# Kernel optimization log

Hardware: AMD Instinct MI355X
Metric: run time of the kernel (lower is better)

The kernel has to match this reference:

```python
import jax, jax.numpy as jnp
import numpy as np

B, T, E, D, N, L, NF = 4, 2048, 512, 512, 16, 4, 2048


def setup_inputs() -> dict:
    key = jax.random.key(0)
    ks = jax.random.split(key, 12)
    r = lambda k, s, sc=1.0: jax.random.normal(k, s, dtype=jnp.float32) * sc
    return {
        "text_emb": r(ks[0], (B, T, E)),
        "W_in": r(ks[1], (E, D), 1.0 / np.sqrt(E).astype(np.float32)),
        "b_in": jnp.zeros((D,), jnp.float32),
        "freq_pe": r(ks[2], (NF, D), 0.02),
        # diagonal-SSM (S4D) params per layer, stacked on leading L axis
        "A_log": r(ks[3], (L, D, N), 0.5),
        "B_ssm": r(ks[4], (L, D, N), 0.5),
        "C_ssm": r(ks[5], (L, D, N), 0.5),
        "log_dt": r(ks[6], (L, D), 0.5) - 4.6,  # dt ~ 0.01
        "D_skip": r(ks[7], (L, D), 0.5),
        "ln_f0_scale": jnp.ones((D,), jnp.float32),
        "ln_f0_bias": jnp.zeros((D,), jnp.float32),
        "W_f0": r(ks[8], (D, 1), 1.0 / np.sqrt(D).astype(np.float32)),
        "b_f0": jnp.zeros((1,), jnp.float32),
        "ln_en_scale": jnp.ones((D,), jnp.float32),
        "ln_en_bias": jnp.zeros((D,), jnp.float32),
        "W_en": r(ks[9], (D, 1), 1.0 / np.sqrt(D).astype(np.float32)),
        "b_en": jnp.zeros((1,), jnp.float32),
    }


def _layernorm(x, scale, bias, eps=1e-5):
    mu = jnp.mean(x, axis=-1, keepdims=True)
    var = jnp.mean(jnp.square(x - mu), axis=-1, keepdims=True)
    return (x - mu) * jax.lax.rsqrt(var + eps) * scale + bias


def _s4_layer(h, A_log, Bm, Cm, log_dt, Dsk):
    # h: [B, T, D]; diagonal SSM with ZOH discretization, scanned over T.
    dt = jnp.exp(log_dt)                 # [D]
    A = -jnp.exp(A_log)                  # [D, N], stable (negative real)
    Abar = jnp.exp(dt[:, None] * A)      # [D, N]
    Bbar = (Abar - 1.0) / A * Bm         # [D, N]
    u_t = jnp.transpose(h, (1, 0, 2))    # [T, B, D]
    x0 = jnp.zeros((h.shape[0], h.shape[2], A.shape[1]), h.dtype)  # [B, D, N]

    def step(x, u):
        x = Abar * x + Bbar * u[..., None]          # [B, D, N]
        y = jnp.einsum('bdn,dn->bd', x, Cm)         # readout
        return x, y

    _, ys = jax.lax.scan(step, x0, u_t)             # ys: [T, B, D]
    y = jnp.transpose(ys, (1, 0, 2)) + Dsk * h      # D skip connection
    return h + jax.nn.gelu(y)                       # residual + activation


def _forward(text_emb, W_in, b_in, freq_pe, A_log, B_ssm, C_ssm, log_dt,
             D_skip, ln_f0_scale, ln_f0_bias, W_f0, b_f0,
             ln_en_scale, ln_en_bias, W_en, b_en):
    x = text_emb @ W_in + b_in                      # [B, T, D]
    Tlen = x.shape[1]
    nf = freq_pe.shape[0]
    if nf >= Tlen:                                  # static-shape crop
        freq = freq_pe[:Tlen]
    else:                                           # static-shape edge pad
        pad = jnp.repeat(freq_pe[-1:], Tlen - nf, axis=0)
        freq = jnp.concatenate([freq_pe, pad], axis=0)
    h = x + freq[None, :, :]
    for l in range(A_log.shape[0]):
        h = _s4_layer(h, A_log[l], B_ssm[l], C_ssm[l], log_dt[l], D_skip[l])
    f0 = (_layernorm(h, ln_f0_scale, ln_f0_bias) @ W_f0 + b_f0)[..., 0]
    en = (_layernorm(h, ln_en_scale, ln_en_bias) @ W_en + b_en)[..., 0]
    return f0, en


def reference(text_emb, W_in, b_in, freq_pe, A_log, B_ssm, C_ssm, log_dt,
              D_skip, ln_f0_scale, ln_f0_bias, W_f0, b_f0,
              ln_en_scale, ln_en_bias, W_en, b_en):
    return _forward(text_emb, W_in, b_in, freq_pe, A_log, B_ssm, C_ssm,
                    log_dt, D_skip, ln_f0_scale, ln_f0_bias, W_f0, b_f0,
                    ln_en_scale, ln_en_bias, W_en, b_en)
```

## Files before the change

### kernel.cpp

```cpp
#include <hip/hip_runtime.h>

#define B_   4
#define T_   2048
#define E_   512
#define D_   512
#define N_   16
#define L_   4
#define TCH  32

typedef __bf16 bf16x8 __attribute__((ext_vector_type(8)));
typedef float  f32x4  __attribute__((ext_vector_type(4)));
typedef float  f32x2  __attribute__((ext_vector_type(2)));
typedef unsigned short us8 __attribute__((ext_vector_type(8)));

__device__ __forceinline__ float us2f(unsigned short u) {
    return __uint_as_float(((unsigned int)u) << 16);
}
__device__ __forceinline__ unsigned short f2us(float f) {
    unsigned int u = __float_as_uint(f);
    unsigned int r = (u + 0x7fffu + ((u >> 16) & 1u)) >> 16;
    return (unsigned short)r;
}
__device__ __forceinline__ float ldin(const void* p, int i, unsigned int f) {
    return f ? ((const float*)p)[i] : us2f(((const unsigned short*)p)[i]);
}
__device__ __forceinline__ unsigned int probe_f32(const void* lnfs) {
    return (((const unsigned int*)lnfs)[0] == 0x3F800000u) ? 1u : 0u;
}
__device__ __forceinline__ f32x2 pk_fma(f32x2 a, f32x2 b, f32x2 c) {
    f32x2 d;
    asm("v_pk_fma_f32 %0, %1, %2, %3" : "=v"(d) : "v"(a), "v"(b), "v"(c));
    return d;
}
template<int CTRL, int RM>
__device__ __forceinline__ f32x2 dpp2(f32x2 v) {
    f32x2 r;
    r[0] = __int_as_float(__builtin_amdgcn_update_dpp(0, __float_as_int(v[0]), CTRL, RM, 0xF, true));
    r[1] = __int_as_float(__builtin_amdgcn_update_dpp(0, __float_as_int(v[1]), CTRL, RM, 0xF, true));
    return r;
}
template<int CTRL>
__device__ __forceinline__ f32x2 mdpp2(f32x2 v) {
    f32x2 r;
    r[0] = __int_as_float(__builtin_amdgcn_mov_dpp(__float_as_int(v[0]), CTRL, 0xF, 0xF, true));
    r[1] = __int_as_float(__builtin_amdgcn_mov_dpp(__float_as_int(v[1]), CTRL, 0xF, 0xF, true));
    return r;
}

#define PA    0
#define PB    32768
#define PC    65536
#define PDT   98304
#define PDSK  100352
#define PLFS  102400
#define PLFB  102912
#define PWF   103424
#define PLES  103936
#define PLEB  104448
#define PWEN  104960
#define PSC   105472
#define PRM_N 105474

#define NB_TEXT 2048
#define NB_PRM  413
#define NB_WT   64
#define NB_S4P  128

__global__ __launch_bounds__(256) void prep_kernel(
    const void* X, const void* Win,
    const void* A_log, const void* B_ssm, const void* C_ssm,
    const void* log_dt, const void* D_skip,
    const void* lnfs, const void* lnfb, const void* Wf0,
    const void* lnes, const void* lneb, const void* Wen,
    const void* bf0, const void* ben,
    unsigned short* __restrict__ textc, unsigned short* __restrict__ Wt,
    float* __restrict__ P, float* __restrict__ P2, float* __restrict__ PW) {
    __shared__ float tile[64 * 65];
    unsigned int f = probe_f32(lnfs);
    int bid = blockIdx.x;
    if (bid < NB_TEXT) {
        int i = (bid * 256 + threadIdx.x) * 8;
        if (f) {
            const float* xf = (const float*)X;
            us8 r;
#pragma unroll
            for (int j = 0; j < 8; j++) r[j] = f2us(xf[i + j]);
            *(us8*)(textc + i) = r;
        } else {
            *(us8*)(textc + i) = *(const us8*)((const unsigned short*)X + i);
        }
    } else if (bid < NB_TEXT + NB_PRM) {
        int i = (bid - NB_TEXT) * 256 + threadIdx.x;
        if      (i < PB)     P[i] = ldin(A_log,  i - PA,   f);
        else if (i < PC)     P[i] = ldin(B_ssm,  i - PB,   f);
        else if (i < PDT)    P[i] = ldin(C_ssm,  i - PC,   f);
        else if (i < PDSK)   P[i] = ldin(log_dt, i - PDT,  f);
        else if (i < PLFS)   P[i] = ldin(D_skip, i - PDSK, f);
        else if (i < PLFB)   P[i] = ldin(lnfs,   i - PLFS, f);
        else if (i < PWF)    P[i] = ldin(lnfb,   i - PLFB, f);
        else if (i < PLES)   P[i] = ldin(Wf0,    i - PWF,  f);
        else if (i < PLEB)   P[i] = ldin(lnes,   i - PLES, f);
        else if (i < PWEN)   P[i] = ldin(lneb,   i - PLEB, f);
        else if (i < PSC)    P[i] = ldin(Wen,    i - PWEN, f);
        else if (i == PSC)     P[i] = ldin(bf0, 0, f);
        else if (i == PSC + 1) P[i] = ldin(ben, 0, f);
    } else if (bid < NB_TEXT + NB_PRM + NB_WT) {
        int tb = bid - (NB_TEXT + NB_PRM);
        int d0 = (tb >> 3) * 64, e0 = (tb & 7) * 64;
        int r = threadIdx.x >> 6, i = threadIdx.x & 63;
#pragma unroll
        for (int k = 0; k < 16; k++) {
            int e = k * 4 + r;
            tile[e * 65 + i] = ldin(Win, (e0 + e) * D_ + d0 + i, f);
        }
        __syncthreads();
#pragma unroll
        for (int k = 0; k < 16; k++) {
            int dd = k * 4 + r;
            Wt[(size_t)(d0 + dd) * E_ + e0 + i] = f2us(tile[i * 65 + dd]);
        }
    } else {
        int i = (bid - (NB_TEXT + NB_PRM + NB_WT)) * 256 + threadIdx.x;
        int n = i & 15;
        int ld = i >> 4;
        float dt = __expf(ldin(log_dt, ld, f));
        float A  = -__expf(ldin(A_log, i, f));
        float Ab = __expf(dt * A);
        float Bb = (Ab - 1.f) / A * ldin(B_ssm, i, f);
        float l2M = 46.166241308446827f * dt * A;
        float M   = exp2f(l2M);
        int base = ld * 32 + n;
        P2[base]      = Ab;
        P2[base + 16] = Bb * ldin(C_ssm, i, f);
        float pw = 1.f;
        size_t pb = ((size_t)ld << 10) + n;
#pragma unroll
        for (int k = 0; k < 33; k++) { PW[pb + (k << 4)] = pw; pw *= M; }
    }
}

__global__ __launch_bounds__(256) void gemm_kernel(const unsigned short* __restrict__ X,
                                                   const unsigned short* __restrict__ Wt,
                                                   const void* __restrict__ freq,
                                                   const void* __restrict__ b_in,
                                                   const void* __restrict__ lnfs,
                                                   float* __restrict__ H) {
    __shared__ unsigned short wlds[64 * 264];
    const unsigned int fl = probe_f32(lnfs);
    const int tid = threadIdx.x;
    const int w  = tid >> 6;
    const int ln = tid & 15;
    const int q  = (tid >> 4) & 3;
    const int d0 = blockIdx.x * 64;
    const int t0 = blockIdx.y * 64;
    const int b  = blockIdx.z;

    f32x4 acc[4];
#pragma unroll
    for (int j = 0; j < 4; j++) { acc[j][0]=0.f; acc[j][1]=0.f; acc[j][2]=0.f; acc[j][3]=0.f; }

    const size_t xbase = ((size_t)b * T_ + t0) * E_;

#pragma unroll
    for (int p = 0; p < 2; ++p) {
        if (p) __syncthreads();
#pragma unroll
        for (int it = 0; it < 8; ++it) {
            int flat = it * 256 + tid;
            int d = flat >> 5;
            int e = (flat & 31) << 3;
            bf16x8 v = *(const bf16x8*)(Wt + (size_t)(d0 + d) * E_ + p * 256 + e);
            *(bf16x8*)(wlds + d * 264 + e) = v;
        }
        __syncthreads();
#pragma unroll
        for (int s = 0; s < 8; ++s) {
            const int eo = s * 32 + q * 8;
            bf16x8 bfr[4];
#pragma unroll
            for (int j = 0; j < 4; j++)
                bfr[j] = *(const bf16x8*)(wlds + (j * 16 + ln) * 264 + eo);
            const int t = w * 16 + ln;
            bf16x8 afr = *(const bf16x8*)(X + xbase + (size_t)t * E_ + p * 256 + eo);
#pragma unroll
            for (int j = 0; j < 4; j++)
                acc[j] = __builtin_amdgcn_mfma_f32_16x16x32_bf16(afr, bfr[j], acc[j], 0, 0, 0);
        }
    }
#pragma unroll
    for (int j = 0; j < 4; j++) {
        int d  = d0 + j * 16 + ln;
        int tb = t0 + w * 16 + q * 4;
        float bi = ldin(b_in, d, fl);
        f32x4 o;
#pragma unroll
        for (int r4 = 0; r4 < 4; r4++)
            o[r4] = acc[j][r4] + ldin(freq, (tb + r4) * D_ + d, fl) + bi;
        *(f32x4*)(H + ((size_t)b * D_ + d) * T_ + tb) = o;
    }
}

__global__ __launch_bounds__(256, 2)
void s4_kernel(float* __restrict__ H, const float* __restrict__ P,
               const float* __restrict__ P2, const float* __restrict__ PW) {
    const int w = threadIdx.x >> 6, lane = threadIdx.x & 63;
    const int d = blockIdx.x;
    const int row = w * D_ + d;
    float* gp = H + (size_t)row * T_ + lane * TCH;

    float u[TCH];
#pragma unroll
    for (int k = 0; k < TCH / 4; k++) {
        f32x4 v = *(const f32x4*)(gp + k * 4);
        u[k * 4] = v[0]; u[k * 4 + 1] = v[1]; u[k * 4 + 2] = v[2]; u[k * 4 + 3] = v[3];
    }

    for (int l = 0; l < L_; ++l) {
        const float* pp  = P2 + (size_t)((l << 9) + d) * 32;
        const float* pwt = PW + ((size_t)((l << 9) + d) << 10);
        f32x2 b[8];
#pragma unroll
        for (int n = 0; n < 8; n++) { b[n][0] = 0.f; b[n][1] = 0.f; }
        {
            f32x2 Ab[8];
#pragma unroll
            for (int n = 0; n < 8; n++) Ab[n] = *(const f32x2*)(pp + 2 * n);
#pragma unroll
            for (int j = 0; j < TCH; j++) {
                f32x2 u2; u2[0] = u[j]; u2[1] = u[j];
#pragma unroll
                for (int n = 0; n < 8; n++) b[n] = pk_fma(Ab[n], b[n], u2);
            }
        }
        {
            f32x2 W[8];
#pragma unroll
            for (int n = 0; n < 8; n++) W[n] = *(const f32x2*)(pwt + 16 + 2 * n);
#pragma unroll
            for (int n = 0; n < 8; n++) b[n] = pk_fma(W[n], mdpp2<0x111>(b[n]), b[n]);
#pragma unroll
            for (int n = 0; n < 8; n++) W[n] = *(const f32x2*)(pwt + 32 + 2 * n);
#pragma unroll
            for (int n = 0; n < 8; n++) b[n] = pk_fma(W[n], mdpp2<0x112>(b[n]), b[n]);
#pragma unroll
            for (int n = 0; n < 8; n++) W[n] = *(const f32x2*)(pwt + 64 + 2 * n);
#pragma unroll
            for (int n = 0; n < 8; n++) b[n] = pk_fma(W[n], mdpp2<0x114>(b[n]), b[n]);
#pragma unroll
            for (int n = 0; n < 8; n++) W[n] = *(const f32x2*)(pwt + 128 + 2 * n);
#pragma unroll
            for (int n = 0; n < 8; n++) b[n] = pk_fma(W[n], mdpp2<0x118>(b[n]), b[n]);
        }
        {
            f32x2 w1[8];
            const float* p1 = pwt + (((lane & 15) + 1) << 4);
#pragma unroll
            for (int n = 0; n < 8; n++) w1[n] = *(const f32x2*)(p1 + 2 * n);
#pragma unroll
            for (int n = 0; n < 8; n++) b[n] = pk_fma(w1[n], dpp2<0x142, 0xA>(b[n]), b[n]);
        }
        {
            f32x2 w2[8];
            const float* p2_ = pwt + (((lane & 31) + 1) << 4);
#pragma unroll
            for (int n = 0; n < 8; n++) w2[n] = *(const f32x2*)(p2_ + 2 * n);
#pragma unroll
            for (int n = 0; n < 8; n++) b[n] = pk_fma(w2[n], dpp2<0x143, 0xC>(b[n]), b[n]);
        }
        f32x2 z[8];
#pragma unroll
        for (int n = 0; n < 8; n++) z[n] = mdpp2<0x138>(b[n]);
        float Dsk = P[PDSK + l * D_ + d];
        f32x2 Ab[8], CB[8];
#pragma unroll
        for (int n = 0; n < 8; n++) Ab[n] = *(const f32x2*)(pp + 2 * n);
#pragma unroll
        for (int n = 0; n < 8; n++) CB[n] = *(const f32x2*)(pp + 16 + 2 * n);
#pragma unroll
        for (int j = 0; j < TCH; j++) {
            float uu = u[j];
            f32x2 u2; u2[0] = uu; u2[1] = uu;
#pragma unroll
            for (int n = 0; n < 8; n++) z[n] = pk_fma(Ab[n], z[n], u2);
            f32x2 ya; ya[0] = 0.f; ya[1] = 0.f;
            f32x2 yb; yb[0] = 0.f; yb[1] = 0.f;
#pragma unroll
            for (int n = 0; n < 8; n += 2) {
                ya = pk_fma(CB[n], z[n], ya);
                yb = pk_fma(CB[n + 1], z[n + 1], yb);
            }
            f32x2 s = ya + yb;
            float y = fmaf(Dsk, uu, s[0] + s[1]);
            float t  = fmaf(0.044715f, y * y * y, y);
            float em = exp2f(-2.30220818f * t);
            float r  = __builtin_amdgcn_rcpf(1.f + em);
            u[j] = fmaf(y, r, uu);
        }
    }
#pragma unroll
    for (int k = 0; k < TCH / 4; k++) {
        f32x4 v;
        v[0] = u[k * 4]; v[1] = u[k * 4 + 1]; v[2] = u[k * 4 + 2]; v[3] = u[k * 4 + 3];
        *(f32x4*)(gp + k * 4) = v;
    }
}

__global__ __launch_bounds__(256) void final_kernel(const float* __restrict__ H,
                                                    const float* __restrict__ P,
                                                    void* __restrict__ out,
                                                    const void* __restrict__ lnfs_raw) {
    __shared__ float red[4][8][32];
    unsigned int f = probe_f32(lnfs_raw);
    int tid = threadIdx.x;
    int w = tid >> 6, lane = tid & 63;
    int tq = lane & 31, dp = lane >> 5;
    int tg = blockIdx.x * 32 + tq;
    int b = tg >> 11, t = tg & (T_ - 1);
    float S1=0.f,S2=0.f,Pf=0.f,Pe=0.f,Cf=0.f,Ce=0.f,Df=0.f,De=0.f;
    const float* hp = H + ((size_t)b * D_) * T_ + t;
#pragma unroll 4
    for (int k = 0; k < 64; k++) {
        int d = w * 128 + 2 * k + dp;
        float hv = hp[(size_t)d * T_];
        float sf = P[PLFS + d], bfv = P[PLFB + d], wf = P[PWF + d];
        float se = P[PLES + d], bev = P[PLEB + d], we = P[PWEN + d];
        S1 += hv; S2 = fmaf(hv, hv, S2);
        float tf = sf * wf, te = se * we;
        Pf = fmaf(hv, tf, Pf); Pe = fmaf(hv, te, Pe);
        Cf += tf; Ce += te;
        Df = fmaf(bfv, wf, Df); De = fmaf(bev, we, De);
    }
    S1 += __shfl_xor(S1, 32); S2 += __shfl_xor(S2, 32);
    Pf += __shfl_xor(Pf, 32); Pe += __shfl_xor(Pe, 32);
    Cf += __shfl_xor(Cf, 32); Ce += __shfl_xor(Ce, 32);
    Df += __shfl_xor(Df, 32); De += __shfl_xor(De, 32);
    if (dp == 0) {
        red[w][0][tq]=S1; red[w][1][tq]=S2; red[w][2][tq]=Pf; red[w][3][tq]=Pe;
        red[w][4][tq]=Cf; red[w][5][tq]=Ce; red[w][6][tq]=Df; red[w][7][tq]=De;
    }
    __syncthreads();
    if (tid < 32) {
        float a[8];
#pragma unroll
        for (int k = 0; k < 8; k++)
            a[k] = red[0][k][tid] + red[1][k][tid] + red[2][k][tid] + red[3][k][tid];
        float mu  = a[0] * (1.f / 512.f);
        float var = a[1] * (1.f / 512.f) - mu * mu;
        float r   = rsqrtf(var + 1e-5f);
        float f0  = r * (a[2] - mu * a[4]) + a[6] + P[PSC + 0];
        float en  = r * (a[3] - mu * a[5]) + a[7] + P[PSC + 1];
        int tg2 = blockIdx.x * 32 + tid;
        if (f) {
            ((float*)out)[tg2]           = f0;
            ((float*)out)[B_ * T_ + tg2] = en;
        } else {
            ((unsigned short*)out)[tg2]           = f2us(f0);
            ((unsigned short*)out)[B_ * T_ + tg2] = f2us(en);
        }
    }
}

extern "C" void kernel_launch(void* const* d_in, const int* in_sizes, int n_in,
                              void* d_out, int out_size, void* d_ws, size_t ws_size,
                              hipStream_t stream) {
    (void)in_sizes; (void)n_in; (void)out_size; (void)ws_size;
    float* ws = (float*)d_ws;
    float* P     = ws;
    float* H     = ws + 105504;
    unsigned short* textc = (unsigned short*)(ws + 4299808);
    unsigned short* Wt    = (unsigned short*)(ws + 6396960);
    float* P2    = ws + 6528032;
    float* PW    = ws + 6593568;

    prep_kernel<<<dim3(NB_TEXT + NB_PRM + NB_WT + NB_S4P), dim3(256), 0, stream>>>(
        d_in[0], d_in[1], d_in[4], d_in[5], d_in[6], d_in[7], d_in[8],
        d_in[9], d_in[10], d_in[11], d_in[13], d_in[14], d_in[15],
        d_in[12], d_in[16], textc, Wt, P, P2, PW);
    gemm_kernel<<<dim3(8, 32, 4), dim3(256), 0, stream>>>(textc, Wt, d_in[3], d_in[2], d_in[9], H);
    s4_kernel<<<dim3(512), dim3(256), 0, stream>>>(H, P, P2, PW);
    final_kernel<<<dim3(256), dim3(256), 0, stream>>>(H, P, d_out, d_in[9]);
}
```

Before: 161.4 us.

## Split S4 state dimension across two waves with LDS readout exchange

The S4 scan kernel now gives each block a single (batch, channel) row handled by two waves. Each wave owns half of the 16 SSM state components, computes partial readouts, and the two partials are combined through shared memory before the GELU/residual step. This doubles wave-level parallelism and halves per-thread state registers. The cost is duplicated u loads and GELU work in both waves, plus two block barriers per layer.

```diff
diff --git a/kernel.cpp b/kernel.cpp
--- a/kernel.cpp
+++ b/kernel.cpp
@@ -200,12 +200,14 @@
     }
 }
 
-__global__ __launch_bounds__(256, 2)
+__global__ __launch_bounds__(128, 4)
 void s4_kernel(float* __restrict__ H, const float* __restrict__ P,
                const float* __restrict__ P2, const float* __restrict__ PW) {
+    __shared__ float xch[32][64][2];
     const int w = threadIdx.x >> 6, lane = threadIdx.x & 63;
-    const int d = blockIdx.x;
-    const int row = w * D_ + d;
+    const int d = blockIdx.x >> 2, b = blockIdx.x & 3;
+    const int row = b * D_ + d;
+    const int no = w << 3;
     float* gp = H + (size_t)row * T_ + lane * TCH;
 
     float u[TCH];
@@ -216,92 +218,96 @@
     }
 
     for (int l = 0; l < L_; ++l) {
-        const float* pp  = P2 + (size_t)((l << 9) + d) * 32;
-        const float* pwt = PW + ((size_t)((l << 9) + d) << 10);
-        f32x2 b[8];
-#pragma unroll
-        for (int n = 0; n < 8; n++) { b[n][0] = 0.f; b[n][1] = 0.f; }
+        const float* pp  = P2 + (size_t)((l << 9) + d) * 32 + no;
+        const float* pwt = PW + (((size_t)((l << 9) + d)) << 10) + no;
+        f32x2 bb[4];
+#pragma unroll
+        for (int n = 0; n < 4; n++) { bb[n][0] = 0.f; bb[n][1] = 0.f; }
+        f32x2 Ab[4];
+#pragma unroll
+        for (int n = 0; n < 4; n++) Ab[n] = *(const f32x2*)(pp + 2 * n);
+#pragma unroll
+        for (int j = 0; j < TCH; j++) {
+            f32x2 u2; u2[0] = u[j]; u2[1] = u[j];
+#pragma unroll
+            for (int n = 0; n < 4; n++) bb[n] = pk_fma(Ab[n], bb[n], u2);
+        }
         {
-            f32x2 Ab[8];
-#pragma unroll
-            for (int n = 0; n < 8; n++) Ab[n] = *(const f32x2*)(pp + 2 * n);
-#pragma unroll
-            for (int j = 0; j < TCH; j++) {
-                f32x2 u2; u2[0] = u[j]; u2[1] = u[j];
-#pragma unroll
-                for (int n = 0; n < 8; n++) b[n] = pk_fma(Ab[n], b[n], u2);
-            }
+            f32x2 W[4];
+#pragma unroll
+            for (int n = 0; n < 4; n++) W[n] = *(const f32x2*)(pwt + 16 + 2 * n);
+#pragma unroll
+            for (int n = 0; n < 4; n++) bb[n] = pk_fma(W[n], mdpp2<0x111>(bb[n]), bb[n]);
+#pragma unroll
+            for (int n = 0; n < 4; n++) W[n] = *(const f32x2*)(pwt + 32 + 2 * n);
+#pragma unroll
+            for (int n = 0; n < 4; n++) bb[n] = pk_fma(W[n], mdpp2<0x112>(bb[n]), bb[n]);
+#pragma unroll
+            for (int n = 0; n < 4; n++) W[n] = *(const f32x2*)(pwt + 64 + 2 * n);
+#pragma unroll
+            for (int n = 0; n < 4; n++) bb[n] = pk_fma(W[n], mdpp2<0x114>(bb[n]), bb[n]);
+#pragma unroll
+            for (int n = 0; n < 4; n++) W[n] = *(const f32x2*)(pwt + 128 + 2 * n);
+#pragma unroll
+            for (int n = 0; n < 4; n++) bb[n] = pk_fma(W[n], mdpp2<0x118>(bb[n]), bb[n]);
         }
         {
-            f32x2 W[8];
-#pragma unroll
-            for (int n = 0; n < 8; n++) W[n] = *(const f32x2*)(pwt + 16 + 2 * n);
-#pragma unroll
-            for (int n = 0; n < 8; n++) b[n] = pk_fma(W[n], mdpp2<0x111>(b[n]), b[n]);
-#pragma unroll
-            for (int n = 0; n < 8; n++) W[n] = *(const f32x2*)(pwt + 32 + 2 * n);
-#pragma unroll
-            for (int n = 0; n < 8; n++) b[n] = pk_fma(W[n], mdpp2<0x112>(b[n]), b[n]);
-#pragma unroll
-            for (int n = 0; n < 8; n++) W[n] = *(const f32x2*)(pwt + 64 + 2 * n);
-#pragma unroll
-            for (int n = 0; n < 8; n++) b[n] = pk_fma(W[n], mdpp2<0x114>(b[n]), b[n]);
-#pragma unroll
-            for (int n = 0; n < 8; n++) W[n] = *(const f32x2*)(pwt + 128 + 2 * n);
-#pragma unroll
-            for (int n = 0; n < 8; n++) b[n] = pk_fma(W[n], mdpp2<0x118>(b[n]), b[n]);
+            f32x2 w1[4];
+            const float* p1 = pwt + (((lane & 15) + 1) << 4);
+#pragma unroll
+            for (int n = 0; n < 4; n++) w1[n] = *(const f32x2*)(p1 + 2 * n);
+#pragma unroll
+            for (int n = 0; n < 4; n++) bb[n] = pk_fma(w1[n], dpp2<0x142, 0xA>(bb[n]), bb[n]);
         }
         {
-            f32x2 w1[8];
-            const float* p1 = pwt + (((lane & 15) + 1) << 4);
-#pragma unroll
-            for (int n = 0; n < 8; n++) w1[n] = *(const f32x2*)(p1 + 2 * n);
-#pragma unroll
-            for (int n = 0; n < 8; n++) b[n] = pk_fma(w1[n], dpp2<0x142, 0xA>(b[n]), b[n]);
-        }
-        {
-            f32x2 w2[8];
+            f32x2 w2[4];
             const float* p2_ = pwt + (((lane & 31) + 1) << 4);
 #pragma unroll
-            for (int n = 0; n < 8; n++) w2[n] = *(const f32x2*)(p2_ + 2 * n);
-#pragma unroll
-            for (int n = 0; n < 8; n++) b[n] = pk_fma(w2[n], dpp2<0x143, 0xC>(b[n]), b[n]);
-        }
-        f32x2 z[8];
-#pragma unroll
-        for (int n = 0; n < 8; n++) z[n] = mdpp2<0x138>(b[n]);
+            for (int n = 0; n < 4; n++) w2[n] = *(const f32x2*)(p2_ + 2 * n);
+#pragma unroll
+            for (int n = 0; n < 4; n++) bb[n] = pk_fma(w2[n], dpp2<0x143, 0xC>(bb[n]), bb[n]);
+        }
+        f32x2 z[4];
+#pragma unroll
+        for (int n = 0; n < 4; n++) z[n] = mdpp2<0x138>(bb[n]);
+        f32x2 CB[4];
+#pragma unroll
+        for (int n = 0; n < 4; n++) CB[n] = *(const f32x2*)(pp + 16 + 2 * n);
+#pragma unroll
+        for (int j = 0; j < TCH; j++) {
+            f32x2 u2; u2[0] = u[j]; u2[1] = u[j];
+#pragma unroll
+            for (int n = 0; n < 4; n++) z[n] = pk_fma(Ab[n], z[n], u2);
+            f32x2 ya; ya[0] = 0.f; ya[1] = 0.f;
+            f32x2 yb; yb[0] = 0.f; yb[1] = 0.f;
+            ya = pk_fma(CB[0], z[0], ya);
+            yb = pk_fma(CB[1], z[1], yb);
+            ya = pk_fma(CB[2], z[2], ya);
+            yb = pk_fma(CB[3], z[3], yb);
+            f32x2 s = ya + yb;
+            xch[j][lane][w] = s[0] + s[1];
+        }
+        __syncthreads();
         float Dsk = P[PDSK + l * D_ + d];
-        f32x2 Ab[8], CB[8];
-#pragma unroll
-        for (int n = 0; n < 8; n++) Ab[n] = *(const f32x2*)(pp + 2 * n);
-#pragma unroll
-        for (int n = 0; n < 8; n++) CB[n] = *(const f32x2*)(pp + 16 + 2 * n);
 #pragma unroll
         for (int j = 0; j < TCH; j++) {
             float uu = u[j];
-            f32x2 u2; u2[0] = uu; u2[1] = uu;
-#pragma unroll
-            for (int n = 0; n < 8; n++) z[n] = pk_fma(Ab[n], z[n], u2);
-            f32x2 ya; ya[0] = 0.f; ya[1] = 0.f;
-            f32x2 yb; yb[0] = 0.f; yb[1] = 0.f;
-#pragma unroll
-            for (int n = 0; n < 8; n += 2) {
-                ya = pk_fma(CB[n], z[n], ya);
-                yb = pk_fma(CB[n + 1], z[n + 1], yb);
-            }
-            f32x2 s = ya + yb;
-            float y = fmaf(Dsk, uu, s[0] + s[1]);
+            f32x2 pr = *(const f32x2*)(&xch[j][lane][0]);
+            float y = fmaf(Dsk, uu, pr[0] + pr[1]);
             float t  = fmaf(0.044715f, y * y * y, y);
             float em = exp2f(-2.30220818f * t);
             float r  = __builtin_amdgcn_rcpf(1.f + em);
             u[j] = fmaf(y, r, uu);
         }
-    }
-#pragma unroll
-    for (int k = 0; k < TCH / 4; k++) {
-        f32x4 v;
-        v[0] = u[k * 4]; v[1] = u[k * 4 + 1]; v[2] = u[k * 4 + 2]; v[3] = u[k * 4 + 3];
-        *(f32x4*)(gp + k * 4) = v;
+        __syncthreads();
+    }
+    if (w == 0) {
+#pragma unroll
+        for (int k = 0; k < TCH / 4; k++) {
+            f32x4 v;
+            v[0] = u[k * 4]; v[1] = u[k * 4 + 1]; v[2] = u[k * 4 + 2]; v[3] = u[k * 4 + 3];
+            *(f32x4*)(gp + k * 4) = v;
+        }
     }
 }
 
@@ -377,6 +383,6 @@
         d_in[9], d_in[10], d_in[11], d_in[13], d_in[14], d_in[15],
         d_in[12], d_in[16], textc, Wt, P, P2, PW);
     gemm_kernel<<<dim3(8, 32, 4), dim3(256), 0, stream>>>(textc, Wt, d_in[3], d_in[2], d_in[9], H);
-    s4_kernel<<<dim3(512), dim3(256), 0, stream>>>(H, P, P2, PW);
+    s4_kernel<<<dim3(2048), dim3(128), 0, stream>>>(H, P, P2, PW);
     final_kernel<<<dim3(256), dim3(256), 0, stream>>>(H, P, d_out, d_in[9]);
 }
```

Result: slower. 183.1 us (+13.4%).
